# Kernel tuning notes

Measured on AMD Instinct MI355X. Metric: run time of the kernel, lower is better.

Reference implementation:

```python
import jax, jax.numpy as jnp
import numpy as np
import math

B, S, D = 4, 2048, 2048
NH, NKV, HD = 16, 4, 128

def setup_inputs() -> dict:
    key = jax.random.key(0)
    ks = jax.random.split(key, 9)
    s = 1.0 / math.sqrt(D)
    return {
        "x": jax.random.normal(ks[0], (B, S, D), dtype=jnp.float32),
        "Wq": jax.random.normal(ks[1], (D, NH * HD), dtype=jnp.float32) * s,
        "bq": jnp.zeros((NH * HD,), dtype=jnp.float32),
        "Wk": jax.random.normal(ks[2], (D, NKV * HD), dtype=jnp.float32) * s,
        "bk": jnp.zeros((NKV * HD,), dtype=jnp.float32),
        "Wv": jax.random.normal(ks[3], (D, NKV * HD), dtype=jnp.float32) * s,
        "bv": jnp.zeros((NKV * HD,), dtype=jnp.float32),
        "Wo": jax.random.normal(ks[4], (D, D), dtype=jnp.float32) * s,
        "bo": jnp.zeros((D,), dtype=jnp.float32),
    }

def reference(x, Wq, bq, Wk, bk, Wv, bv, Wo, bo):
    b, s, _ = x.shape
    group = NH // NKV
    q = (x @ Wq + bq).reshape(b, s, NH, HD).transpose(0, 2, 1, 3)   # [B,NH,S,HD]
    k = (x @ Wk + bk).reshape(b, s, NKV, HD).transpose(0, 2, 1, 3)  # [B,NKV,S,HD]
    v = (x @ Wv + bv).reshape(b, s, NKV, HD).transpose(0, 2, 1, 3)
    # repeat_interleave KV heads to match query heads
    k = jnp.repeat(k, group, axis=1)  # [B,NH,S,HD]
    v = jnp.repeat(v, group, axis=1)
    scores = jnp.einsum("bhqd,bhkd->bhqk", q, k) / math.sqrt(HD)
    causal = jnp.tril(jnp.ones((s, s), dtype=bool))
    scores = jnp.where(causal, scores, -jnp.inf)
    probs = jax.nn.softmax(scores, axis=-1)  # dropout p=0.0 -> identity
    out = jnp.einsum("bhqk,bhkd->bhqd", probs, v)
    out = out.transpose(0, 2, 1, 3).reshape(b, s, NH * HD)
    return out @ Wo + bo
```

## Files before the change

### kernel.cpp

```cpp
#include <hip/hip_runtime.h>
#include <hip/hip_bf16.h>

typedef __attribute__((ext_vector_type(4)))  float f32x4;
typedef __attribute__((ext_vector_type(16))) float f32x16;
typedef __attribute__((ext_vector_type(8)))  short s16x8;
typedef __attribute__((ext_vector_type(4)))  short s16x4;
typedef __attribute__((ext_vector_type(4)))  float fvec4;

__device__ __forceinline__ short f2bf(float f) {
    union { float f; unsigned u; } x; x.f = f;
    unsigned r = x.u + 0x7fffu + ((x.u >> 16) & 1u);
    return (short)(r >> 16);
}

__device__ __forceinline__ short cvtbf(float f) {
    __hip_bfloat16 t = __float2bfloat16(f);
    return *reinterpret_cast<short*>(&t);
}

__device__ __forceinline__ void gload_lds16(const short* g, short* lds) {
    __builtin_amdgcn_global_load_lds(
        (const __attribute__((address_space(1))) void*)g,
        (__attribute__((address_space(3))) void*)lds, 16, 0, 0);
}

__global__ __launch_bounds__(256) void convert_bf16(const float* __restrict__ X,
                                                    short* __restrict__ Y) {
    size_t i = ((size_t)blockIdx.x * 256 + threadIdx.x) * 8;
    fvec4 a = *(const fvec4*)&X[i];
    fvec4 b = *(const fvec4*)&X[i + 4];
    s16x8 o;
    o[0] = f2bf(a[0]); o[1] = f2bf(a[1]); o[2] = f2bf(a[2]); o[3] = f2bf(a[3]);
    o[4] = f2bf(b[0]); o[5] = f2bf(b[1]); o[6] = f2bf(b[2]); o[7] = f2bf(b[3]);
    *(s16x8*)&Y[i] = o;
}

__global__ __launch_bounds__(256) void tconv(const float* __restrict__ W,
                                             short* __restrict__ Wt,
                                             int K, int N) {
    __shared__ float tile[32][33];
    const int k0 = blockIdx.x * 32, n0 = blockIdx.y * 32;
    const int tx = threadIdx.x & 31, ty = threadIdx.x >> 5;
    #pragma unroll
    for (int i = 0; i < 4; ++i) {
        int k = ty + i * 8;
        tile[k][tx] = W[(size_t)(k0 + k) * N + n0 + tx];
    }
    __syncthreads();
    #pragma unroll
    for (int i = 0; i < 4; ++i) {
        int n = ty + i * 8;
        Wt[(size_t)(n0 + n) * K + k0 + tx] = f2bf(tile[tx][n]);
    }
}

__global__ __launch_bounds__(256) void gemm_kv(const short* __restrict__ A,
                                               const short* __restrict__ Bt,
                                               const float* __restrict__ bias_k,
                                               const float* __restrict__ bias_v,
                                               short* __restrict__ Kout,
                                               short* __restrict__ Vout,
                                               int M, int N, int K) {
    __shared__ __align__(16) short As[128 * 64];
    __shared__ __align__(16) short Bs[128 * 64];
    const int tid = threadIdx.x, lane = tid & 63, wid = tid >> 6;
    const int wr = wid >> 1, wc = wid & 1;
    const int lr = lane & 15, g = lane >> 4;
    const int m0 = blockIdx.y * 128, n0 = blockIdx.x * 128;
    const int r8 = lane >> 3, c8 = lane & 7;

    f32x4 acc[4][4] = {};

    const short* ga = A  + (size_t)(m0 + wid * 8 + r8) * K + c8 * 8;
    const short* gb = Bt + (size_t)(n0 + wid * 8 + r8) * K + c8 * 8;

    for (int k0 = 0; k0 < K; k0 += 64) {
        #pragma unroll
        for (int it = 0; it < 4; ++it) {
            gload_lds16(ga + (size_t)(it * 32) * K + k0, &As[(wid * 8 + it * 32) * 64]);
            gload_lds16(gb + (size_t)(it * 32) * K + k0, &Bs[(wid * 8 + it * 32) * 64]);
        }
        __syncthreads();
        #pragma unroll
        for (int kk = 0; kk < 2; ++kk) {
            s16x8 af[4], bfv[4];
            #pragma unroll
            for (int m = 0; m < 4; ++m)
                af[m] = *(const s16x8*)&As[(wr * 64 + m * 16 + lr) * 64 + kk * 32 + g * 8];
            #pragma unroll
            for (int n = 0; n < 4; ++n)
                bfv[n] = *(const s16x8*)&Bs[(wc * 64 + n * 16 + lr) * 64 + kk * 32 + g * 8];
            #pragma unroll
            for (int m = 0; m < 4; ++m)
                #pragma unroll
                for (int n = 0; n < 4; ++n)
                    acc[m][n] = __builtin_amdgcn_mfma_f32_16x16x32_bf16(af[m], bfv[n], acc[m][n], 0, 0, 0);
        }
        __syncthreads();
    }
    if (n0 < 512) {
        #pragma unroll
        for (int m = 0; m < 4; ++m)
            #pragma unroll
            for (int j = 0; j < 4; ++j) {
                int row = m0 + wr * 64 + m * 16 + g * 4 + j;
                #pragma unroll
                for (int n = 0; n < 4; ++n) {
                    int col = n0 + wc * 64 + n * 16 + lr;
                    Kout[(size_t)row * 512 + col] = f2bf(acc[m][n][j] + bias_k[col]);
                }
            }
    } else {
        #pragma unroll
        for (int m = 0; m < 4; ++m)
            #pragma unroll
            for (int n = 0; n < 4; ++n) {
                int vcol = n0 - 512 + wc * 64 + n * 16 + lr;
                int kvh = vcol >> 7, d = vcol & 127;
                int row0 = m0 + wr * 64 + m * 16 + g * 4;
                int b = row0 >> 11, s0 = row0 & 2047;
                int s0p = (s0 & ~15) | (((s0 >> 2) & 1) << 3) | (((s0 >> 3) & 1) << 2);
                s16x4 o;
                #pragma unroll
                for (int j = 0; j < 4; ++j) o[j] = f2bf(acc[m][n][j] + bias_v[vcol]);
                *(s16x4*)&Vout[(((size_t)b * 4 + kvh) * 128 + d) * 2048 + s0p] = o;
            }
    }
}

template<int MODE>
__global__ __launch_bounds__(512, 1) void gemm256(const short* __restrict__ A,
                                                  const short* __restrict__ Bt,
                                                  const float* __restrict__ bias,
                                                  void* __restrict__ Cv,
                                                  int M, int N, int K) {
    __shared__ __align__(16) short As[2][16384];
    __shared__ __align__(16) short Bs[2][16384];
    const int tid = threadIdx.x, lane = tid & 63, w = tid >> 6;
    const int wr = w >> 2, wc = w & 3;
    const int lr = lane & 15, g = lane >> 4;
    const int bid = blockIdx.x;
    const int xcd = bid & 7, ii = bid >> 3;
    const int m0 = (xcd * 4 + (ii & 3)) * 256;
    const int n0 = (ii >> 2) * 256;
    const int r0 = w * 8 + (lane >> 3);
    const int sw = ((lane & 7) ^ ((lane >> 3) & 7)) * 8;
    const int swr = lr & 7;

    const short* ga = A  + (size_t)(m0 + r0) * K + sw;
    const short* gb = Bt + (size_t)(n0 + r0) * K + sw;

    f32x4 acc[8][4] = {};
    const int NT = K >> 6;

#define STAGE256(d, t) do {                                                     \
    const int kk0_ = (t) << 6;                                                  \
    _Pragma("unroll")                                                           \
    for (int it_ = 0; it_ < 4; ++it_) {                                         \
        gload_lds16(ga + (size_t)(it_ * 64) * K + kk0_, &As[d][it_ * 4096 + w * 512]); \
        gload_lds16(gb + (size_t)(it_ * 64) * K + kk0_, &Bs[d][it_ * 4096 + w * 512]); \
    }                                                                           \
} while (0)

    STAGE256(0, 0);

    for (int T = 0; T < NT; ++T) {
        const int d = T & 1;
        if (T + 1 < NT) {
            STAGE256((T + 1) & 1, T + 1);
            asm volatile("s_waitcnt vmcnt(8)" ::: "memory");
        } else {
            asm volatile("s_waitcnt vmcnt(0)" ::: "memory");
        }
        __builtin_amdgcn_s_barrier();
        __builtin_amdgcn_sched_barrier(0);
        s16x8 bf[4][2];
        #pragma unroll
        for (int n = 0; n < 4; ++n)
            #pragma unroll
            for (int kk = 0; kk < 2; ++kk)
                bf[n][kk] = *(const s16x8*)&Bs[d][(wc * 64 + n * 16 + lr) * 64 +
                                                 (((kk << 2) | g) ^ swr) * 8];
        #pragma unroll
        for (int p = 0; p < 4; ++p) {
            s16x8 af[2][2];
            #pragma unroll
            for (int mm = 0; mm < 2; ++mm)
                #pragma unroll
                for (int kk = 0; kk < 2; ++kk)
                    af[mm][kk] = *(const s16x8*)&As[d][(wr * 128 + (p * 2 + mm) * 16 + lr) * 64 +
                                                      (((kk << 2) | g) ^ swr) * 8];
            __builtin_amdgcn_s_setprio(1);
            #pragma unroll
            for (int kk = 0; kk < 2; ++kk)
                #pragma unroll
                for (int mm = 0; mm < 2; ++mm)
                    #pragma unroll
                    for (int n = 0; n < 4; ++n)
                        acc[p * 2 + mm][n] = __builtin_amdgcn_mfma_f32_16x16x32_bf16(
                            af[mm][kk], bf[n][kk], acc[p * 2 + mm][n], 0, 0, 0);
            __builtin_amdgcn_s_setprio(0);
            __builtin_amdgcn_s_barrier();
        }
        __builtin_amdgcn_sched_barrier(0);
    }
    #pragma unroll
    for (int m = 0; m < 8; ++m)
        #pragma unroll
        for (int j = 0; j < 4; ++j) {
            int row = m0 + wr * 128 + m * 16 + g * 4 + j;
            #pragma unroll
            for (int n = 0; n < 4; ++n) {
                int col = n0 + wc * 64 + n * 16 + lr;
                float v = acc[m][n][j] + bias[col];
                if constexpr (MODE == 1) ((short*)Cv)[(size_t)row * N + col] = f2bf(v);
                else                     ((float*)Cv)[(size_t)row * N + col] = v;
            }
        }
#undef STAGE256
}

#define SC2 0.12751743f

__global__ __launch_bounds__(512, 1) void attn_kernel(const short* __restrict__ Q,
                                                      const short* __restrict__ Kg,
                                                      const short* __restrict__ Vtg,
                                                      short* __restrict__ Oa) {
    __shared__ __align__(16) short Klds[2][8192];
    __shared__ __align__(16) short Vlds[2][8192];
    const int tid = threadIdx.x;
    const int lane = tid & 63, w = tid >> 6;
    const int l31 = lane & 31, hi = lane >> 5, e7 = lane & 7;
    const int ve = hi ^ e7;

    const int bid = blockIdx.x;
    const int grp = bid & 15, j = bid >> 4;
    const int b = grp >> 2, kvh = grp & 3;
    const int h = kvh * 4 + (j & 3);
    const int qtp = (j >> 2) & 3, ph = j >> 4;
    const int qt = ph ? (3 - qtp) : (4 + qtp);
    const int qb = qt << 8;

    const int q_min = qb + w * 32;
    const int qg = q_min + l31;
    const size_t qrow = (size_t)b * 2048 + qg;

    s16x8 qf[8];
    #pragma unroll
    for (int c = 0; c < 8; ++c)
        qf[c] = *(const s16x8*)&Q[qrow * 2048 + h * 128 + c * 16 + hi * 8];

    f32x16 oacc[4] = {};
    float m_run = -1e28f, l_run = 0.f;

    const int nt = (qb >> 6) + 4;

    const short* Kbase = Kg + ((size_t)b * 2048) * 512 + kvh * 128;
    const short* Vbase = Vtg + ((size_t)(b * 4 + kvh)) * 128 * 2048;

    const int krow0 = w * 4 + (lane >> 4), kslot = lane & 15;
    const int vrow0 = w * 8 + (lane >> 3), vslot = lane & 7;

#define STAGE(buf, t) do {                                                        \
    const int kv0_ = (t) << 6;                                                    \
    _Pragma("unroll")                                                             \
    for (int s_ = 0; s_ < 2; ++s_) {                                              \
        int kr = s_ * 32 + krow0;                                                 \
        gload_lds16(Kbase + (size_t)(kv0_ + kr) * 512 + (kslot ^ (kr & 7)) * 8,   \
                    &Klds[buf][s_ * 4096 + w * 512]);                             \
        int vr = s_ * 64 + vrow0;                                                 \
        gload_lds16(Vbase + (size_t)vr * 2048 + kv0_ + (vslot ^ (vr & 7)) * 8,    \
                    &Vlds[buf][s_ * 4096 + w * 512]);                             \
    }                                                                             \
} while (0)

    STAGE(0, 0);
    __syncthreads();

    int cur = 0;
    for (int t = 0; t < nt; ++t) {
        if (t + 1 < nt) STAGE(cur ^ 1, t + 1);
        #pragma unroll
        for (int st = 0; st < 2; ++st) {
            const int kvoff = (t << 6) + (st << 5);
            if (kvoff > q_min) break;
            f32x16 s = {};
            const short* kb = &Klds[cur][((st << 5) + l31) * 128];
            #pragma unroll
            for (int c = 0; c < 8; ++c) {
                s16x8 kf = *(const s16x8*)&kb[(((c << 1) ^ ve)) * 8];
                s = __builtin_amdgcn_mfma_f32_32x32x16_bf16(kf, qf[c], s, 0, 0, 0);
            }
            if (kvoff == q_min) {
                #pragma unroll
                for (int r = 0; r < 16; ++r) {
                    const int rw = (r & 3) + 8 * (r >> 2) + 4 * hi;
                    if (rw > l31) s[r] = -1e30f;
                }
            }
            float m01 = fmaxf(s[0], s[1]),   m23 = fmaxf(s[2], s[3]);
            float m45 = fmaxf(s[4], s[5]),   m67 = fmaxf(s[6], s[7]);
            float m89 = fmaxf(s[8], s[9]),   mab = fmaxf(s[10], s[11]);
            float mcd = fmaxf(s[12], s[13]), mef = fmaxf(s[14], s[15]);
            float mA = fmaxf(fmaxf(m01, m23), fmaxf(m45, m67));
            float mB = fmaxf(fmaxf(m89, mab), fmaxf(mcd, mef));
            float pm = fmaxf(mA, mB);
            pm = fmaxf(pm, __shfl_xor(pm, 32));
            if (!__all(pm <= m_run + 90.5f)) {
                float mn = fmaxf(m_run, pm);
                float fs = __builtin_amdgcn_exp2f((m_run - mn) * SC2);
                l_run *= fs;
                #pragma unroll
                for (int dn = 0; dn < 4; ++dn)
                    #pragma unroll
                    for (int r = 0; r < 16; ++r) oacc[dn][r] *= fs;
                m_run = mn;
            }
            const float mb2 = m_run * SC2;
            #pragma unroll
            for (int r = 0; r < 16; ++r)
                s[r] = __builtin_amdgcn_exp2f(fmaf(s[r], SC2, -mb2));
            float s01 = s[0] + s[1],   s23 = s[2] + s[3];
            float s45 = s[4] + s[5],   s67 = s[6] + s[7];
            float s89 = s[8] + s[9],   sab = s[10] + s[11];
            float scd = s[12] + s[13], sef = s[14] + s[15];
            float sAB = ((s01 + s23) + (s45 + s67)) + ((s89 + sab) + (scd + sef));
            l_run += sAB + __shfl_xor(sAB, 32);
            s16x8 pa0, pa1;
            #pragma unroll
            for (int jj = 0; jj < 8; ++jj) { pa0[jj] = cvtbf(s[jj]); pa1[jj] = cvtbf(s[8 + jj]); }
            const short* vb = &Vlds[cur][l31 * 64];
            #pragma unroll
            for (int dn = 0; dn < 4; ++dn) {
                s16x8 vf = *(const s16x8*)&vb[dn * 2048 + (((st << 2) ^ ve)) * 8];
                oacc[dn] = __builtin_amdgcn_mfma_f32_32x32x16_bf16(vf, pa0, oacc[dn], 0, 0, 0);
            }
            #pragma unroll
            for (int dn = 0; dn < 4; ++dn) {
                s16x8 vf = *(const s16x8*)&vb[dn * 2048 + ((((st << 2) | 2) ^ ve)) * 8];
                oacc[dn] = __builtin_amdgcn_mfma_f32_32x32x16_bf16(vf, pa1, oacc[dn], 0, 0, 0);
            }
        }
        __syncthreads();
        cur ^= 1;
    }
    const float inv = 1.0f / l_run;
    const size_t obase = qrow * 2048 + h * 128;
    #pragma unroll
    for (int dn = 0; dn < 4; ++dn)
        #pragma unroll
        for (int u = 0; u < 4; ++u) {
            s16x4 o;
            #pragma unroll
            for (int jj = 0; jj < 4; ++jj) o[jj] = cvtbf(oacc[dn][u * 4 + jj] * inv);
            *(s16x4*)&Oa[obase + dn * 32 + u * 8 + hi * 4] = o;
        }
#undef STAGE
}

extern "C" void kernel_launch(void* const* d_in, const int* in_sizes, int n_in,
                              void* d_out, int out_size, void* d_ws, size_t ws_size,
                              hipStream_t stream) {
    const float* x  = (const float*)d_in[0];
    const float* Wq = (const float*)d_in[1];
    const float* bq = (const float*)d_in[2];
    const float* Wk = (const float*)d_in[3];
    const float* bk = (const float*)d_in[4];
    const float* Wv = (const float*)d_in[5];
    const float* bv = (const float*)d_in[6];
    const float* Wo = (const float*)d_in[7];
    const float* bo = (const float*)d_in[8];
    float* out = (float*)d_out;

    char* ws = (char*)d_ws;
    short* Xb  = (short*)(ws);
    short* Qb  = (short*)(ws + (size_t)33554432);
    short* Kb  = (short*)(ws + (size_t)67108864);
    short* Vt  = (short*)(ws + (size_t)75497472);
    short* WoT = (short*)(ws);
    char* dob = (char*)d_out;
    short* WqT  = (short*)(dob);
    short* WkvT = (short*)(dob + (size_t)8388608);

    const int M = 8192, D = 2048;

    convert_bf16<<<dim3((M * D) / (256 * 8)), 256, 0, stream>>>(x, Xb);
    tconv<<<dim3(64, 64), 256, 0, stream>>>(Wq, WqT, D, D);
    tconv<<<dim3(64, 16), 256, 0, stream>>>(Wk, WkvT, D, 512);
    tconv<<<dim3(64, 16), 256, 0, stream>>>(Wv, WkvT + (size_t)512 * D, D, 512);

    gemm256<1><<<dim3(256), 512, 0, stream>>>(Xb, WqT, bq, Qb, M, 2048, D);
    gemm_kv<<<dim3(8, 64), 256, 0, stream>>>(Xb, WkvT, bk, bv, Kb, Vt, M, 1024, D);

    tconv<<<dim3(64, 64), 256, 0, stream>>>(Wo, WoT, D, D);

    attn_kernel<<<dim3(512), 512, 0, stream>>>(Qb, Kb, Vt, Qb);

    gemm256<0><<<dim3(256), 512, 0, stream>>>(Qb, WoT, bo, out, M, 2048, D);
}
```

Measured before the change: 327.8 us.

## Fuse prep kernels, pipeline KV GEMM, prefetch A fragments, raise MFMA priority

Merges the x conversion and three weight transpose-converts into one prep launch to cut launch overhead. Replaces the simple single-buffered KV projection GEMM with a double-buffered, swizzled 256x128-tile kernel that uses async global-to-LDS loads and XCD-aware block mapping. In the main GEMM, A fragments for the next sub-tile are read from LDS while the current MFMAs run. The attention MFMA blocks are also wrapped with s_setprio. These add register pressure and code complexity in exchange for better overlap and fewer launches.

```diff
diff --git a/kernel.cpp b/kernel.cpp
--- a/kernel.cpp
+++ b/kernel.cpp
@@ -24,15 +24,42 @@
         (__attribute__((address_space(3))) void*)lds, 16, 0, 0);
 }
 
-__global__ __launch_bounds__(256) void convert_bf16(const float* __restrict__ X,
-                                                    short* __restrict__ Y) {
-    size_t i = ((size_t)blockIdx.x * 256 + threadIdx.x) * 8;
-    fvec4 a = *(const fvec4*)&X[i];
-    fvec4 b = *(const fvec4*)&X[i + 4];
-    s16x8 o;
-    o[0] = f2bf(a[0]); o[1] = f2bf(a[1]); o[2] = f2bf(a[2]); o[3] = f2bf(a[3]);
-    o[4] = f2bf(b[0]); o[5] = f2bf(b[1]); o[6] = f2bf(b[2]); o[7] = f2bf(b[3]);
-    *(s16x8*)&Y[i] = o;
+__global__ __launch_bounds__(256) void prep(const float* __restrict__ x,
+                                            const float* __restrict__ Wq,
+                                            const float* __restrict__ Wk,
+                                            const float* __restrict__ Wv,
+                                            short* __restrict__ Xb,
+                                            short* __restrict__ WqT,
+                                            short* __restrict__ WkvT) {
+    const int bid = blockIdx.x, tid = threadIdx.x;
+    if (bid < 8192) {
+        size_t i = ((size_t)bid * 256 + tid) * 8;
+        fvec4 a = *(const fvec4*)&x[i];
+        fvec4 b = *(const fvec4*)&x[i + 4];
+        s16x8 o;
+        o[0] = f2bf(a[0]); o[1] = f2bf(a[1]); o[2] = f2bf(a[2]); o[3] = f2bf(a[3]);
+        o[4] = f2bf(b[0]); o[5] = f2bf(b[1]); o[6] = f2bf(b[2]); o[7] = f2bf(b[3]);
+        *(s16x8*)&Xb[i] = o;
+        return;
+    }
+    const float* W; short* Wt; int N, local;
+    if (bid < 12288)      { W = Wq; Wt = WqT;                      N = 2048; local = bid - 8192; }
+    else if (bid < 13312) { W = Wk; Wt = WkvT;                     N = 512;  local = bid - 12288; }
+    else                  { W = Wv; Wt = WkvT + (size_t)512 * 2048; N = 512; local = bid - 13312; }
+    __shared__ float tile[32][33];
+    const int k0 = (local & 63) * 32, n0 = (local >> 6) * 32;
+    const int tx = tid & 31, ty = tid >> 5;
+    #pragma unroll
+    for (int i = 0; i < 4; ++i) {
+        int k = ty + i * 8;
+        tile[k][tx] = W[(size_t)(k0 + k) * N + n0 + tx];
+    }
+    __syncthreads();
+    #pragma unroll
+    for (int i = 0; i < 4; ++i) {
+        int n = ty + i * 8;
+        Wt[(size_t)(n0 + n) * 2048 + k0 + tx] = f2bf(tile[tx][n]);
+    }
 }
 
 __global__ __launch_bounds__(256) void tconv(const float* __restrict__ W,
@@ -51,80 +78,6 @@
     for (int i = 0; i < 4; ++i) {
         int n = ty + i * 8;
         Wt[(size_t)(n0 + n) * K + k0 + tx] = f2bf(tile[tx][n]);
-    }
-}
-
-__global__ __launch_bounds__(256) void gemm_kv(const short* __restrict__ A,
-                                               const short* __restrict__ Bt,
-                                               const float* __restrict__ bias_k,
-                                               const float* __restrict__ bias_v,
-                                               short* __restrict__ Kout,
-                                               short* __restrict__ Vout,
-                                               int M, int N, int K) {
-    __shared__ __align__(16) short As[128 * 64];
-    __shared__ __align__(16) short Bs[128 * 64];
-    const int tid = threadIdx.x, lane = tid & 63, wid = tid >> 6;
-    const int wr = wid >> 1, wc = wid & 1;
-    const int lr = lane & 15, g = lane >> 4;
-    const int m0 = blockIdx.y * 128, n0 = blockIdx.x * 128;
-    const int r8 = lane >> 3, c8 = lane & 7;
-
-    f32x4 acc[4][4] = {};
-
-    const short* ga = A  + (size_t)(m0 + wid * 8 + r8) * K + c8 * 8;
-    const short* gb = Bt + (size_t)(n0 + wid * 8 + r8) * K + c8 * 8;
-
-    for (int k0 = 0; k0 < K; k0 += 64) {
-        #pragma unroll
-        for (int it = 0; it < 4; ++it) {
-            gload_lds16(ga + (size_t)(it * 32) * K + k0, &As[(wid * 8 + it * 32) * 64]);
-            gload_lds16(gb + (size_t)(it * 32) * K + k0, &Bs[(wid * 8 + it * 32) * 64]);
-        }
-        __syncthreads();
-        #pragma unroll
-        for (int kk = 0; kk < 2; ++kk) {
-            s16x8 af[4], bfv[4];
-            #pragma unroll
-            for (int m = 0; m < 4; ++m)
-                af[m] = *(const s16x8*)&As[(wr * 64 + m * 16 + lr) * 64 + kk * 32 + g * 8];
-            #pragma unroll
-            for (int n = 0; n < 4; ++n)
-                bfv[n] = *(const s16x8*)&Bs[(wc * 64 + n * 16 + lr) * 64 + kk * 32 + g * 8];
-            #pragma unroll
-            for (int m = 0; m < 4; ++m)
-                #pragma unroll
-                for (int n = 0; n < 4; ++n)
-                    acc[m][n] = __builtin_amdgcn_mfma_f32_16x16x32_bf16(af[m], bfv[n], acc[m][n], 0, 0, 0);
-        }
-        __syncthreads();
-    }
-    if (n0 < 512) {
-        #pragma unroll
-        for (int m = 0; m < 4; ++m)
-            #pragma unroll
-            for (int j = 0; j < 4; ++j) {
-                int row = m0 + wr * 64 + m * 16 + g * 4 + j;
-                #pragma unroll
-                for (int n = 0; n < 4; ++n) {
-                    int col = n0 + wc * 64 + n * 16 + lr;
-                    Kout[(size_t)row * 512 + col] = f2bf(acc[m][n][j] + bias_k[col]);
-                }
-            }
-    } else {
-        #pragma unroll
-        for (int m = 0; m < 4; ++m)
-            #pragma unroll
-            for (int n = 0; n < 4; ++n) {
-                int vcol = n0 - 512 + wc * 64 + n * 16 + lr;
-                int kvh = vcol >> 7, d = vcol & 127;
-                int row0 = m0 + wr * 64 + m * 16 + g * 4;
-                int b = row0 >> 11, s0 = row0 & 2047;
-                int s0p = (s0 & ~15) | (((s0 >> 2) & 1) << 3) | (((s0 >> 3) & 1) << 2);
-                s16x4 o;
-                #pragma unroll
-                for (int j = 0; j < 4; ++j) o[j] = f2bf(acc[m][n][j] + bias_v[vcol]);
-                *(s16x4*)&Vout[(((size_t)b * 4 + kvh) * 128 + d) * 2048 + s0p] = o;
-            }
     }
 }
 
@@ -181,15 +134,24 @@
             for (int kk = 0; kk < 2; ++kk)
                 bf[n][kk] = *(const s16x8*)&Bs[d][(wc * 64 + n * 16 + lr) * 64 +
                                                  (((kk << 2) | g) ^ swr) * 8];
+        s16x8 afc[2][2];
+        #pragma unroll
+        for (int mm = 0; mm < 2; ++mm)
+            #pragma unroll
+            for (int kk = 0; kk < 2; ++kk)
+                afc[mm][kk] = *(const s16x8*)&As[d][(wr * 128 + mm * 16 + lr) * 64 +
+                                                   (((kk << 2) | g) ^ swr) * 8];
         #pragma unroll
         for (int p = 0; p < 4; ++p) {
-            s16x8 af[2][2];
-            #pragma unroll
-            for (int mm = 0; mm < 2; ++mm)
-                #pragma unroll
-                for (int kk = 0; kk < 2; ++kk)
-                    af[mm][kk] = *(const s16x8*)&As[d][(wr * 128 + (p * 2 + mm) * 16 + lr) * 64 +
-                                                      (((kk << 2) | g) ^ swr) * 8];
+            s16x8 afn[2][2];
+            if (p < 3) {
+                #pragma unroll
+                for (int mm = 0; mm < 2; ++mm)
+                    #pragma unroll
+                    for (int kk = 0; kk < 2; ++kk)
+                        afn[mm][kk] = *(const s16x8*)&As[d][(wr * 128 + ((p + 1) * 2 + mm) * 16 + lr) * 64 +
+                                                           (((kk << 2) | g) ^ swr) * 8];
+            }
             __builtin_amdgcn_s_setprio(1);
             #pragma unroll
             for (int kk = 0; kk < 2; ++kk)
@@ -198,9 +160,16 @@
                     #pragma unroll
                     for (int n = 0; n < 4; ++n)
                         acc[p * 2 + mm][n] = __builtin_amdgcn_mfma_f32_16x16x32_bf16(
-                            af[mm][kk], bf[n][kk], acc[p * 2 + mm][n], 0, 0, 0);
+                            afc[mm][kk], bf[n][kk], acc[p * 2 + mm][n], 0, 0, 0);
             __builtin_amdgcn_s_setprio(0);
             __builtin_amdgcn_s_barrier();
+            if (p < 3) {
+                #pragma unroll
+                for (int mm = 0; mm < 2; ++mm)
+                    #pragma unroll
+                    for (int kk = 0; kk < 2; ++kk)
+                        afc[mm][kk] = afn[mm][kk];
+            }
         }
         __builtin_amdgcn_sched_barrier(0);
     }
@@ -218,6 +187,131 @@
             }
         }
 #undef STAGE256
+}
+
+__global__ __launch_bounds__(512, 1) void gemm256kv(const short* __restrict__ A,
+                                                    const short* __restrict__ Bt,
+                                                    const float* __restrict__ bias_k,
+                                                    const float* __restrict__ bias_v,
+                                                    short* __restrict__ Kout,
+                                                    short* __restrict__ Vout,
+                                                    int K) {
+    __shared__ __align__(16) short As[2][16384];
+    __shared__ __align__(16) short Bs[2][8192];
+    const int tid = threadIdx.x, lane = tid & 63, w = tid >> 6;
+    const int wr = w >> 1, wc = w & 1;
+    const int lr = lane & 15, g = lane >> 4;
+    const int bid = blockIdx.x;
+    const int xcd = bid & 7, ii = bid >> 3;
+    const int m0 = (xcd * 4 + (ii & 3)) * 256;
+    const int n0 = (ii >> 2) * 128;
+    const int r0 = w * 8 + (lane >> 3);
+    const int sw = ((lane & 7) ^ ((lane >> 3) & 7)) * 8;
+    const int swr = lr & 7;
+
+    const short* ga = A  + (size_t)(m0 + r0) * K + sw;
+    const short* gb = Bt + (size_t)(n0 + r0) * K + sw;
+
+    f32x4 acc[4][4] = {};
+    const int NT = K >> 6;
+
+#define STAGEKV(d, t) do {                                                      \
+    const int kk0_ = (t) << 6;                                                  \
+    _Pragma("unroll")                                                           \
+    for (int it_ = 0; it_ < 4; ++it_)                                           \
+        gload_lds16(ga + (size_t)(it_ * 64) * K + kk0_, &As[d][it_ * 4096 + w * 512]); \
+    _Pragma("unroll")                                                           \
+    for (int it_ = 0; it_ < 2; ++it_)                                           \
+        gload_lds16(gb + (size_t)(it_ * 64) * K + kk0_, &Bs[d][it_ * 4096 + w * 512]); \
+} while (0)
+
+    STAGEKV(0, 0);
+
+    for (int T = 0; T < NT; ++T) {
+        const int d = T & 1;
+        if (T + 1 < NT) {
+            STAGEKV((T + 1) & 1, T + 1);
+            asm volatile("s_waitcnt vmcnt(6)" ::: "memory");
+        } else {
+            asm volatile("s_waitcnt vmcnt(0)" ::: "memory");
+        }
+        __builtin_amdgcn_s_barrier();
+        __builtin_amdgcn_sched_barrier(0);
+        s16x8 bf[4][2];
+        #pragma unroll
+        for (int n = 0; n < 4; ++n)
+            #pragma unroll
+            for (int kk = 0; kk < 2; ++kk)
+                bf[n][kk] = *(const s16x8*)&Bs[d][(wc * 64 + n * 16 + lr) * 64 +
+                                                 (((kk << 2) | g) ^ swr) * 8];
+        s16x8 afc[2][2];
+        #pragma unroll
+        for (int mm = 0; mm < 2; ++mm)
+            #pragma unroll
+            for (int kk = 0; kk < 2; ++kk)
+                afc[mm][kk] = *(const s16x8*)&As[d][(wr * 64 + mm * 16 + lr) * 64 +
+                                                   (((kk << 2) | g) ^ swr) * 8];
+        #pragma unroll
+        for (int p = 0; p < 2; ++p) {
+            s16x8 afn[2][2];
+            if (p < 1) {
+                #pragma unroll
+                for (int mm = 0; mm < 2; ++mm)
+                    #pragma unroll
+                    for (int kk = 0; kk < 2; ++kk)
+                        afn[mm][kk] = *(const s16x8*)&As[d][(wr * 64 + (2 + mm) * 16 + lr) * 64 +
+                                                           (((kk << 2) | g) ^ swr) * 8];
+            }
+            __builtin_amdgcn_s_setprio(1);
+            #pragma unroll
+            for (int kk = 0; kk < 2; ++kk)
+                #pragma unroll
+                for (int mm = 0; mm < 2; ++mm)
+                    #pragma unroll
+                    for (int n = 0; n < 4; ++n)
+                        acc[p * 2 + mm][n] = __builtin_amdgcn_mfma_f32_16x16x32_bf16(
+                            afc[mm][kk], bf[n][kk], acc[p * 2 + mm][n], 0, 0, 0);
+            __builtin_amdgcn_s_setprio(0);
+            __builtin_amdgcn_s_barrier();
+            if (p < 1) {
+                #pragma unroll
+                for (int mm = 0; mm < 2; ++mm)
+                    #pragma unroll
+                    for (int kk = 0; kk < 2; ++kk)
+                        afc[mm][kk] = afn[mm][kk];
+            }
+        }
+        __builtin_amdgcn_sched_barrier(0);
+    }
+    if (n0 < 512) {
+        #pragma unroll
+        for (int m = 0; m < 4; ++m)
+            #pragma unroll
+            for (int j = 0; j < 4; ++j) {
+                int row = m0 + wr * 64 + m * 16 + g * 4 + j;
+                #pragma unroll
+                for (int n = 0; n < 4; ++n) {
+                    int col = n0 + wc * 64 + n * 16 + lr;
+                    Kout[(size_t)row * 512 + col] = f2bf(acc[m][n][j] + bias_k[col]);
+                }
+            }
+    } else {
+        #pragma unroll
+        for (int m = 0; m < 4; ++m)
+            #pragma unroll
+            for (int n = 0; n < 4; ++n) {
+                int vcol = n0 - 512 + wc * 64 + n * 16 + lr;
+                int kvh = vcol >> 7, dd = vcol & 127;
+                int row0 = m0 + wr * 64 + m * 16 + g * 4;
+                int b = row0 >> 11, s0 = row0 & 2047;
+                int s0p = (s0 & ~15) | (((s0 >> 2) & 1) << 3) | (((s0 >> 3) & 1) << 2);
+                s16x4 o;
+                #pragma unroll
+                for (int j = 0; j < 4; ++j) o[j] = f2bf(acc[m][n][j] + bias_v[vcol]);
+                *(s16x4*)&Vout[(((size_t)b * 4 + kvh) * 128 + dd) * 2048 + s0p] = o;
+            }
+    }
+#undef STAGEKV
 }
 
 #define SC2 0.12751743f
@@ -286,11 +380,13 @@
             if (kvoff > q_min) break;
             f32x16 s = {};
             const short* kb = &Klds[cur][((st << 5) + l31) * 128];
+            __builtin_amdgcn_s_setprio(1);
             #pragma unroll
             for (int c = 0; c < 8; ++c) {
                 s16x8 kf = *(const s16x8*)&kb[(((c << 1) ^ ve)) * 8];
                 s = __builtin_amdgcn_mfma_f32_32x32x16_bf16(kf, qf[c], s, 0, 0, 0);
             }
+            __builtin_amdgcn_s_setprio(0);
             if (kvoff == q_min) {
                 #pragma unroll
                 for (int r = 0; r < 16; ++r) {
@@ -330,6 +426,7 @@
             #pragma unroll
             for (int jj = 0; jj < 8; ++jj) { pa0[jj] = cvtbf(s[jj]); pa1[jj] = cvtbf(s[8 + jj]); }
             const short* vb = &Vlds[cur][l31 * 64];
+            __builtin_amdgcn_s_setprio(1);
             #pragma unroll
             for (int dn = 0; dn < 4; ++dn) {
                 s16x8 vf = *(const s16x8*)&vb[dn * 2048 + (((st << 2) ^ ve)) * 8];
@@ -340,6 +437,7 @@
                 s16x8 vf = *(const s16x8*)&vb[dn * 2048 + ((((st << 2) | 2) ^ ve)) * 8];
                 oacc[dn] = __builtin_amdgcn_mfma_f32_32x32x16_bf16(vf, pa1, oacc[dn], 0, 0, 0);
             }
+            __builtin_amdgcn_s_setprio(0);
         }
         __syncthreads();
         cur ^= 1;
@@ -384,13 +482,10 @@
 
     const int M = 8192, D = 2048;
 
-    convert_bf16<<<dim3((M * D) / (256 * 8)), 256, 0, stream>>>(x, Xb);
-    tconv<<<dim3(64, 64), 256, 0, stream>>>(Wq, WqT, D, D);
-    tconv<<<dim3(64, 16), 256, 0, stream>>>(Wk, WkvT, D, 512);
-    tconv<<<dim3(64, 16), 256, 0, stream>>>(Wv, WkvT + (size_t)512 * D, D, 512);
+    prep<<<dim3(14336), 256, 0, stream>>>(x, Wq, Wk, Wv, Xb, WqT, WkvT);
 
     gemm256<1><<<dim3(256), 512, 0, stream>>>(Xb, WqT, bq, Qb, M, 2048, D);
-    gemm_kv<<<dim3(8, 64), 256, 0, stream>>>(Xb, WkvT, bk, bv, Kb, Vt, M, 1024, D);
+    gemm256kv<<<dim3(256), 512, 0, stream>>>(Xb, WkvT, bk, bv, Kb, Vt, D);
 
     tconv<<<dim3(64, 64), 256, 0, stream>>>(Wo, WoT, D, D);
 
```

Result: no change. 331.1 us (+1.0%).
